# Performance work log

Hardware: AMD Instinct MI355X
Metric: run time of the kernel (lower is better)

The kernel has to match this reference:

```python
import jax, jax.numpy as jnp
import numpy as np

T, B, C, H, W = 4, 8, 256, 16, 16
HEADS = 8
N = H * W
TN = T * N
DH = C // HEADS
DECAY = 0.25

# STE quantizer: fwd round(clamp(x,0,1)); bwd passes grad only where 0<=x<=1
@jax.custom_vjp
def quant1(x):
    return jnp.round(jnp.clip(x, 0.0, 1.0))

def _q_fwd(x):
    return quant1(x), x

def _q_bwd(x, g):
    return (jnp.where((x < 0) | (x > 1), 0.0, g),)

quant1.defvjp(_q_fwd, _q_bwd)

def lif(x):
    # x: [T, ...]; sequential LIF membrane decay + quantize over leading (time) axis
    def step(carry, xt):
        mem_old, spike = carry
        mem = (mem_old - jax.lax.stop_gradient(spike) * 0.5) * DECAY + xt
        s = quant1(mem)
        return (mem, s), s
    z = jnp.zeros_like(x[0])
    _, out = jax.lax.scan(step, (z, z), x)
    return out

def bn1d(x, gamma, beta, mean, var):
    # eval-mode BatchNorm1d over channel axis 1 of [B, Ch, L]
    inv = jax.lax.rsqrt(var + 1e-5)
    return (x - mean[None, :, None]) * (gamma * inv)[None, :, None] + beta[None, :, None]

def _rel_pos_index():
    coords = np.stack(np.meshgrid(np.arange(T), np.arange(H), np.arange(W), indexing='ij'))  # [3,T,H,W]
    cf = coords.reshape(3, -1)                      # [3, TN]
    rc = (cf[:, :, None] - cf[:, None, :]).transpose(1, 2, 0).copy()  # [TN, TN, 3]
    rc[:, :, 0] += T - 1
    rc[:, :, 1] += H - 1
    rc[:, :, 2] += W - 1
    rc[:, :, 0] *= (2 * H - 1) * (2 * W - 1)
    rc[:, :, 1] *= (2 * W - 1)
    return rc.sum(-1)                               # [TN, TN] ints

def _mask():
    m = np.ones((TN, TN), np.float32)
    for t in range(T - 1):
        m[t * N:(t + 1) * N, (t + 1) * N:] = 0.0
    return m

_RPI = jnp.asarray(_rel_pos_index().reshape(-1))
_MASK = jnp.asarray(_mask())


def setup_inputs() -> dict:
    key = jax.random.key(0)
    ks = jax.random.split(key, 13)
    bias_rows = (2 * T - 1) * (2 * H - 1) * (2 * W - 1)
    return {
        'x': jax.random.normal(ks[0], (T, B, C, H, W), jnp.float32),
        'w_qkv': jax.random.normal(ks[1], (3 * C, C), jnp.float32) * 0.05,
        'qkv_gamma': jax.random.uniform(ks[2], (3 * C,), jnp.float32, 0.5, 1.5),
        'qkv_beta': jax.random.normal(ks[3], (3 * C,), jnp.float32) * 0.1,
        'qkv_mean': jax.random.normal(ks[4], (3 * C,), jnp.float32) * 0.1,
        'qkv_var': jax.random.uniform(ks[5], (3 * C,), jnp.float32, 0.5, 1.5),
        'bias_table': jax.random.normal(ks[6], (bias_rows, HEADS), jnp.float32) * 0.02,
        'w_proj': jax.random.normal(ks[7], (C, C), jnp.float32) * 0.05,
        'b_proj': jax.random.normal(ks[8], (C,), jnp.float32) * 0.02,
        'proj_gamma': jax.random.uniform(ks[9], (C,), jnp.float32, 0.5, 1.5),
        'proj_beta': jax.random.normal(ks[10], (C,), jnp.float32) * 0.1,
        'proj_mean': jax.random.normal(ks[11], (C,), jnp.float32) * 0.1,
        'proj_var': jax.random.uniform(ks[12], (C,), jnp.float32, 0.5, 1.5),
    }


def reference(x, w_qkv, qkv_gamma, qkv_beta, qkv_mean, qkv_var, bias_table,
              w_proj, b_proj, proj_gamma, proj_beta, proj_mean, proj_var):
    # flatten spatial, then raw reshape [T,B,C,N] -> [B,C,T*N] (as in torch source)
    xf = x.reshape(T, B, C, N).reshape(B, C, T * N)
    # 1x1 conv == channel matmul, then eval BN
    qkv = jnp.einsum('oc,bcl->bol', w_qkv, xf)
    qkv = bn1d(qkv, qkv_gamma, qkv_beta, qkv_mean, qkv_var)
    qkv = qkv.reshape(B, 3 * C, T, N).transpose(2, 0, 1, 3)  # [T,B,3C,N]
    qkv = lif(qkv).transpose(1, 0, 3, 2)                      # [B,T,N,3C]
    q, k, v = jnp.split(qkv, 3, axis=-1)                      # each [B,T,N,C]

    def to_heads(z):  # b t n (h d) -> b h (t n) d
        return z.reshape(B, T, N, HEADS, DH).transpose(0, 3, 1, 2, 4).reshape(B, HEADS, TN, DH)
    q, k, v = map(to_heads, (q, k, v))

    bias = bias_table[_RPI].reshape(TN, TN, HEADS).transpose(2, 0, 1)  # [h,TN,TN]
    attn = jnp.einsum('bhnd,bhmd->bhnm', q, k) + bias[None]
    attn = attn * _MASK[None, None]                                     # block upper-triangle mask
    o = jnp.einsum('bhnm,bhmd->bhnd', attn, v) * 0.125                  # [B,h,TN,d]

    o = o.transpose(0, 2, 1, 3).reshape(B, TN, C).reshape(B, T, N, C).transpose(1, 0, 3, 2)  # [T,B,C,N]
    o = lif(o)
    o = o.transpose(1, 2, 0, 3).reshape(B, C, T * N)          # [B,C,TN]
    o = jnp.einsum('oc,bcl->bol', w_proj, o) + b_proj[None, :, None]
    o = bn1d(o, proj_gamma, proj_beta, proj_mean, proj_var)
    o = o.reshape(B, C, T, N).transpose(2, 0, 1, 3).reshape(T, B, C, H, W)
    return lif(o)
```

## Files before the change

kernel.cpp:

```cpp
#include <hip/hip_runtime.h>
#include <stdint.h>
#include <math.h>

constexpr int T_ = 4;
constexpr int B_ = 8;
constexpr int C_ = 256;
constexpr int N_ = 256;
constexpr int TN_ = 1024;
constexpr int NH_ = 8;
constexpr int O3_ = 768;
constexpr int BIAS_ROWS_ = 6727;

__device__ __constant__ int TI_OF[10] = {0,1,1,2,2,2,3,3,3,3};
__device__ __constant__ int TJ_OF[10] = {0,0,1,0,1,2,0,1,2,3};

__device__ __forceinline__ float quant1f(float m) {
    return rintf(fminf(fmaxf(m, 0.0f), 1.0f));
}

__global__ __launch_bounds__(256) void k1_qkv_gemm(
    const float* __restrict__ x, const float* __restrict__ w,
    const float* __restrict__ gamma, const float* __restrict__ beta,
    const float* __restrict__ mean, const float* __restrict__ var,
    float* __restrict__ out)
{
    __shared__ float At[32][36];
    __shared__ float Bt[32][132];
    const int b = blockIdx.z;
    const int oBase = blockIdx.y * 32;
    const int lBase = blockIdx.x * 128;
    const int tid = threadIdx.x;
    const int tx = tid & 31;
    const int ty = tid >> 5;
    const float* xb = x + (size_t)b * C_ * TN_;

    float acc[4][4];
#pragma unroll
    for (int i = 0; i < 4; ++i)
#pragma unroll
        for (int j = 0; j < 4; ++j) acc[i][j] = 0.0f;

    const int a_row0 = tid >> 4, a_k2 = (tid & 15) * 2;
    const int b_kk0 = tid >> 5, b_c4 = (tid & 31) * 4;

    for (int kc = 0; kc < 8; ++kc) {
        const int k0 = kc * 32;
#pragma unroll
        for (int r = 0; r < 2; ++r) {
            const int row = a_row0 + 16 * r;
            const float2 v = *(const float2*)&w[(size_t)(oBase + row) * C_ + k0 + a_k2];
            At[a_k2][row] = v.x;
            At[a_k2 + 1][row] = v.y;
        }
#pragma unroll
        for (int r = 0; r < 4; ++r) {
            const int kk = b_kk0 + 8 * r;
            const float4 v = *(const float4*)&xb[(size_t)(k0 + kk) * TN_ + lBase + b_c4];
            *(float4*)&Bt[kk][b_c4] = v;
        }
        __syncthreads();
#pragma unroll
        for (int cc = 0; cc < 32; ++cc) {
            float a[4], bb[4];
            *(float4*)&a[0] = *(const float4*)&At[cc][ty * 4];
            *(float4*)&bb[0] = *(const float4*)&Bt[cc][tx * 4];
#pragma unroll
            for (int i = 0; i < 4; ++i)
#pragma unroll
                for (int j = 0; j < 4; ++j) acc[i][j] += a[i] * bb[j];
        }
        __syncthreads();
    }

#pragma unroll
    for (int i = 0; i < 4; ++i) {
        const int o = oBase + ty * 4 + i;
        const float inv = 1.0f / sqrtf(var[o] + 1e-5f);
        const float g = gamma[o] * inv;
        const float mn = mean[o], bt = beta[o];
        float4 st;
        st.x = (acc[i][0] - mn) * g + bt;
        st.y = (acc[i][1] - mn) * g + bt;
        st.z = (acc[i][2] - mn) * g + bt;
        st.w = (acc[i][3] - mn) * g + bt;
        *(float4*)&out[((size_t)b * O3_ + o) * TN_ + lBase + tx * 4] = st;
    }
}

__global__ __launch_bounds__(256) void k2_lif_pack(
    const float* __restrict__ qkv,
    uint32_t* __restrict__ qb, uint32_t* __restrict__ kb, uint32_t* __restrict__ vb)
{
    const int n = threadIdx.x;
    const int g = blockIdx.x;
    const int b = blockIdx.y;
    const int dq = blockIdx.z;
    const int which = g >> 3, h = g & 7;
    uint32_t* dstw = (which == 0) ? qb : (which == 1) ? kb : vb;
    uint8_t* dst = (uint8_t*)dstw;
    const float* src = qkv + ((size_t)b * O3_ + g * 32 + dq * 8) * TN_;

    float memv[8];
#pragma unroll
    for (int d = 0; d < 8; ++d) memv[d] = 0.0f;
    uint32_t prev = 0;

    for (int t = 0; t < T_; ++t) {
        uint32_t bits = 0;
#pragma unroll
        for (int d = 0; d < 8; ++d) {
            const float xv = src[(size_t)d * TN_ + t * N_ + n];
            const float m = (memv[d] - 0.5f * (float)((prev >> d) & 1u)) * 0.25f + xv;
            memv[d] = m;
            const float s = quant1f(m);
            bits |= ((uint32_t)s) << d;
        }
        prev = bits;
        dst[4 * (((size_t)b * NH_ + h) * TN_ + t * N_ + n) + dq] = (uint8_t)bits;
    }
}

__global__ __launch_bounds__(256) void k3_tgp(
    const uint32_t* __restrict__ kb, const uint32_t* __restrict__ vb,
    int* __restrict__ Pt)
{
    __shared__ uint64_t ks[32][4];
    __shared__ uint64_t vs[32][4];
    const int t = blockIdx.x;
    const int bh = blockIdx.y;
    const int tid = threadIdx.x;
    const int q = tid >> 6, lane = tid & 63;
    const int j = t * N_ + q * 64 + lane;

    const uint32_t kw = kb[(size_t)bh * TN_ + j];
    const uint32_t vw = vb[(size_t)bh * TN_ + j];
#pragma unroll
    for (int d = 0; d < 32; ++d) {
        const uint64_t mk = __ballot((kw >> d) & 1u);
        const uint64_t mv = __ballot((vw >> d) & 1u);
        if (lane == 0) { ks[d][q] = mk; vs[d][q] = mv; }
    }
    __syncthreads();

    const int d = tid & 31;
#pragma unroll
    for (int s = 0; s < 4; ++s) {
        const int d2 = (tid >> 5) + 8 * s;
        int p = 0;
#pragma unroll
        for (int w = 0; w < 4; ++w) p += __popcll(ks[d2][w] & vs[d][w]);
        Pt[(size_t)(bh * 4 + t) * 1024 + d2 * 32 + d] = p;
    }
}

__global__ __launch_bounds__(256) void k3_cum(
    const int* __restrict__ Pt, float* __restrict__ Gf)
{
    const int bh = blockIdx.x;
    const int tid = threadIdx.x;
#pragma unroll
    for (int r = 0; r < 4; ++r) {
        const int idx = tid + 256 * r;
        int cum = 0;
#pragma unroll
        for (int t = 0; t < T_; ++t) {
            cum += Pt[(size_t)(bh * 4 + t) * 1024 + idx];
            Gf[(size_t)(bh * 4 + t) * 1024 + idx] = (float)cum;
        }
    }
}

__global__ __launch_bounds__(256) void k3_bias_gemm(
    const uint32_t* __restrict__ vb, const float* __restrict__ bias_table,
    float* __restrict__ p0, float* __restrict__ p1,
    float* __restrict__ p2, float* __restrict__ p3)
{
    __shared__ float sbl[544];
    __shared__ float At[32][36];
    __shared__ float Bt[32][132];

    const int z = blockIdx.z;
    const int h = z / 10;
    const int p = z % 10;
    const int ti = TI_OF[p], tj = TJ_OF[p];
    const int dt = ti - tj;
    const int iT = blockIdx.y;
    const int nBase = blockIdx.x * 128;
    const int tid = threadIdx.x;

    const int base = 3363 + 961 * dt + 62 * iT - 480;
    for (int s = tid; s < 544; s += 256) {
        const int gidx = base + s;
        sbl[s] = (gidx >= 0 && gidx < BIAS_ROWS_) ? bias_table[(size_t)gidx * NH_ + h] : 0.0f;
    }

    const int ty2 = tid >> 4, tx16 = tid & 15;

    const int il0 = ty2 * 2;
    const int sRowBase = 480 + 31 * (il0 >> 4) + (il0 & 15) - tx16;

    const int n8 = tx16 * 8;
    const int nS = nBase + n8;
    const int bS = nS >> 5, d0S = nS & 31;
    const uint32_t* vbw = vb + ((size_t)bS * NH_ + h) * TN_ + tj * 256 + ty2;

    const int tyc = tid >> 5, txc = tid & 31;
    const int nA = nBase + txc * 4;
    const int bA = nA >> 5, dA = nA & 31;

    float acc[4][4];
#pragma unroll
    for (int i = 0; i < 4; ++i)
#pragma unroll
        for (int j = 0; j < 4; ++j) acc[i][j] = 0.0f;

    __syncthreads();

    for (int kc = 0; kc < 8; ++kc) {
#pragma unroll
        for (int r1 = 0; r1 < 2; ++r1) {
            const int s0 = sRowBase - 31 * (kc * 2 + r1);
            float2 av;
            av.x = sbl[s0];
            av.y = sbl[s0 + 1];
            At[tx16 + 16 * r1][il0] = av.x;
            At[tx16 + 16 * r1][il0 + 1] = av.y;
        }
#pragma unroll
        for (int r = 0; r < 2; ++r) {
            const uint32_t wd = vbw[kc * 32 + 16 * r];
            float4 b0, b1;
            b0.x = (float)((wd >> d0S) & 1u);
            b0.y = (float)((wd >> (d0S + 1)) & 1u);
            b0.z = (float)((wd >> (d0S + 2)) & 1u);
            b0.w = (float)((wd >> (d0S + 3)) & 1u);
            b1.x = (float)((wd >> (d0S + 4)) & 1u);
            b1.y = (float)((wd >> (d0S + 5)) & 1u);
            b1.z = (float)((wd >> (d0S + 6)) & 1u);
            b1.w = (float)((wd >> (d0S + 7)) & 1u);
            *(float4*)&Bt[ty2 + 16 * r][n8] = b0;
            *(float4*)&Bt[ty2 + 16 * r][n8 + 4] = b1;
        }
        __syncthreads();
#pragma unroll
        for (int cc = 0; cc < 32; ++cc) {
            float a[4], bb[4];
            *(float4*)&a[0] = *(const float4*)&At[cc][tyc * 4];
            *(float4*)&bb[0] = *(const float4*)&Bt[cc][txc * 4];
#pragma unroll
            for (int i = 0; i < 4; ++i)
#pragma unroll
                for (int j = 0; j < 4; ++j) acc[i][j] += a[i] * bb[j];
        }
        __syncthreads();
    }

    float* plane = (tj == 0) ? p0 : (tj == 1) ? p1 : (tj == 2) ? p2 : p3;
    const int nrows = (4 - tj) * 256;
    const int cA = h * 32 + dA;
#pragma unroll
    for (int r = 0; r < 4; ++r) {
        const int rowL = dt * 256 + iT * 32 + tyc * 4 + r;
        float4 s0;
        s0.x = acc[r][0]; s0.y = acc[r][1]; s0.z = acc[r][2]; s0.w = acc[r][3];
        *(float4*)&plane[((size_t)bA * nrows + rowL) * 256 + cA] = s0;
    }
}

__global__ __launch_bounds__(256) void k4_lif2(
    const uint32_t* __restrict__ qb, const float* __restrict__ Gf,
    const float* __restrict__ p0, const float* __restrict__ p1,
    const float* __restrict__ p2, const float* __restrict__ p3,
    uint32_t* __restrict__ s2c)
{
    const int c = threadIdx.x;
    const int n = blockIdx.x;
    const int b = blockIdx.y;
    const int lane = c & 63;
    const int h = c >> 5, d = c & 31;
    const int bh = b * NH_ + h;
    const uint32_t* qbh = qb + (size_t)bh * TN_;

    float memv = 0.0f, spk = 0.0f;
    for (int t = 0; t < T_; ++t) {
        const int l = t * N_ + n;
        const uint32_t q = qbh[l];
        const float* g = Gf + (size_t)(bh * 4 + t) * 1024 + d;
        float v = 0.0f;
#pragma unroll
        for (int d2 = 0; d2 < 32; ++d2)
            v += ((q >> d2) & 1u) ? g[d2 * 32] : 0.0f;
        v += p0[((size_t)b * 1024 + l) * 256 + c];
        if (t >= 1) v += p1[((size_t)b * 768 + (l - 256)) * 256 + c];
        if (t >= 2) v += p2[((size_t)b * 512 + (l - 512)) * 256 + c];
        if (t >= 3) v += p3[((size_t)b * 256 + (l - 768)) * 256 + c];
        const float m = (memv - 0.5f * spk) * 0.25f + 0.125f * v;
        memv = m;
        const float s = quant1f(m);
        spk = s;
        const uint64_t mask = __ballot(s != 0.0f);
        if (lane == 0)
            s2c[((size_t)b * TN_ + l) * 8 + (c >> 5)] = (uint32_t)mask;
        else if (lane == 32)
            s2c[((size_t)b * TN_ + l) * 8 + (c >> 5)] = (uint32_t)(mask >> 32);
    }
}

__global__ __launch_bounds__(256) void k5_proj_lif(
    const uint32_t* __restrict__ s2c, const float* __restrict__ w,
    const float* __restrict__ bp,
    const float* __restrict__ gamma, const float* __restrict__ beta,
    const float* __restrict__ mean, const float* __restrict__ var,
    float* __restrict__ out)
{
    __shared__ float At[128][36];
    __shared__ uint32_t Sw[128 * 9];
    const int nBase = blockIdx.x * 32;
    const int oBase = blockIdx.y * 32;
    const int b = blockIdx.z;
    const int tid = threadIdx.x;
    const int tx = tid & 31;
    const int ty = tid >> 5;

#pragma unroll
    for (int j = 0; j < 4; ++j) {
        const int fidx = tid * 4 + j;
        const int lp = fidx >> 3, wsel = fidx & 7;
        const int t = lp >> 5, nn = lp & 31;
        Sw[lp * 9 + wsel] = s2c[((size_t)b * TN_ + t * 256 + nBase + nn) * 8 + wsel];
    }

    const int a_row = tid >> 3, a_kq = (tid & 7) * 16;

    float acc[4][4];
#pragma unroll
    for (int r = 0; r < 4; ++r)
#pragma unroll
        for (int t = 0; t < 4; ++t) acc[r][t] = 0.0f;

    for (int half = 0; half < 2; ++half) {
        if (half) __syncthreads();
#pragma unroll
        for (int j = 0; j < 4; ++j) {
            const float4 v = *(const float4*)&w[(size_t)(oBase + a_row) * C_ + half * 128 + a_kq + 4 * j];
            At[a_kq + 4 * j][a_row] = v.x;
            At[a_kq + 4 * j + 1][a_row] = v.y;
            At[a_kq + 4 * j + 2][a_row] = v.z;
            At[a_kq + 4 * j + 3][a_row] = v.w;
        }
        __syncthreads();

        for (int ks = 0; ks < 4; ++ks) {
            uint32_t wr[4];
#pragma unroll
            for (int t = 0; t < 4; ++t)
                wr[t] = Sw[(t * 32 + tx) * 9 + half * 4 + ks];
#pragma unroll
            for (int u = 0; u < 32; ++u) {
                float a[4];
                *(float4*)&a[0] = *(const float4*)&At[ks * 32 + u][ty * 4];
                float bv[4];
#pragma unroll
                for (int t = 0; t < 4; ++t) bv[t] = (float)((wr[t] >> u) & 1u);
#pragma unroll
                for (int r = 0; r < 4; ++r)
#pragma unroll
                    for (int t = 0; t < 4; ++t) acc[r][t] += a[r] * bv[t];
            }
        }
    }

#pragma unroll
    for (int r = 0; r < 4; ++r) {
        const int o = oBase + ty * 4 + r;
        const float inv = 1.0f / sqrtf(var[o] + 1e-5f);
        const float g = gamma[o] * inv;
        const float mn = mean[o], bt = beta[o], bpo = bp[o];
        float memv = 0.0f, spk = 0.0f;
#pragma unroll
        for (int t = 0; t < 4; ++t) {
            const float val = ((acc[r][t] + bpo) - mn) * g + bt;
            const float m = (memv - 0.5f * spk) * 0.25f + val;
            memv = m;
            const float s = quant1f(m);
            spk = s;
            out[(((size_t)t * B_ + b) * C_ + o) * N_ + nBase + tx] = s;
        }
    }
}

extern "C" void kernel_launch(void* const* d_in, const int* in_sizes, int n_in,
                              void* d_out, int out_size, void* d_ws, size_t ws_size,
                              hipStream_t stream)
{
    const float* x          = (const float*)d_in[0];
    const float* w_qkv      = (const float*)d_in[1];
    const float* qkv_gamma  = (const float*)d_in[2];
    const float* qkv_beta   = (const float*)d_in[3];
    const float* qkv_mean   = (const float*)d_in[4];
    const float* qkv_var    = (const float*)d_in[5];
    const float* bias_table = (const float*)d_in[6];
    const float* w_proj     = (const float*)d_in[7];
    const float* b_proj     = (const float*)d_in[8];
    const float* proj_gamma = (const float*)d_in[9];
    const float* proj_beta  = (const float*)d_in[10];
    const float* proj_mean  = (const float*)d_in[11];
    const float* proj_var   = (const float*)d_in[12];
    float* out = (float*)d_out;

    char* ws = (char*)d_ws;
    float*    qkv_bn = (float*)(ws + 0);
    float*    part0  = (float*)(ws + 1048576);
    float*    part1  = (float*)(ws + 9437184);
    float*    part2  = (float*)(ws + 15728640);
    float*    part3  = (float*)(ws + 19922944);
    float*    Gf     = (float*)(ws + 25165824);
    int*      Pt     = (int*)  (ws + 26214400);
    uint32_t* s2c    = (uint32_t*)(ws + 33554432);
    uint32_t* qbits  = (uint32_t*)(ws + 50331648);
    uint32_t* kbits  = (uint32_t*)(ws + 50593792);
    uint32_t* vbits  = (uint32_t*)(ws + 50855936);

    k1_qkv_gemm<<<dim3(8, 24, 8), 256, 0, stream>>>(
        x, w_qkv, qkv_gamma, qkv_beta, qkv_mean, qkv_var, qkv_bn);

    k2_lif_pack<<<dim3(24, 8, 4), 256, 0, stream>>>(qkv_bn, qbits, kbits, vbits);

    k3_tgp<<<dim3(4, 64), 256, 0, stream>>>(kbits, vbits, Pt);

    k3_cum<<<dim3(64), 256, 0, stream>>>(Pt, Gf);

    k3_bias_gemm<<<dim3(2, 8, 80), 256, 0, stream>>>(
        vbits, bias_table, part0, part1, part2, part3);

    k4_lif2<<<dim3(256, 8), 256, 0, stream>>>(
        qbits, Gf, part0, part1, part2, part3, s2c);

    k5_proj_lif<<<dim3(8, 8, 8), 256, 0, stream>>>(
        s2c, w_proj, b_proj, proj_gamma, proj_beta, proj_mean, proj_var, out);
}
```

Baseline: 213.8 us.

## Retile QKV and proj GEMMs, fold cumulative sum into LIF2 kernel

```diff
diff --git a/kernel.cpp b/kernel.cpp
--- a/kernel.cpp
+++ b/kernel.cpp
@@ -24,19 +24,19 @@
     const float* __restrict__ mean, const float* __restrict__ var,
     float* __restrict__ out)
 {
-    __shared__ float At[32][36];
+    __shared__ float At[32][68];
     __shared__ float Bt[32][132];
     const int b = blockIdx.z;
-    const int oBase = blockIdx.y * 32;
+    const int oBase = blockIdx.y * 64;
     const int lBase = blockIdx.x * 128;
     const int tid = threadIdx.x;
     const int tx = tid & 31;
     const int ty = tid >> 5;
     const float* xb = x + (size_t)b * C_ * TN_;
 
-    float acc[4][4];
-#pragma unroll
-    for (int i = 0; i < 4; ++i)
+    float acc[8][4];
+#pragma unroll
+    for (int i = 0; i < 8; ++i)
 #pragma unroll
         for (int j = 0; j < 4; ++j) acc[i][j] = 0.0f;
 
@@ -46,7 +46,7 @@
     for (int kc = 0; kc < 8; ++kc) {
         const int k0 = kc * 32;
 #pragma unroll
-        for (int r = 0; r < 2; ++r) {
+        for (int r = 0; r < 4; ++r) {
             const int row = a_row0 + 16 * r;
             const float2 v = *(const float2*)&w[(size_t)(oBase + row) * C_ + k0 + a_k2];
             At[a_k2][row] = v.x;
@@ -61,11 +61,12 @@
         __syncthreads();
 #pragma unroll
         for (int cc = 0; cc < 32; ++cc) {
-            float a[4], bb[4];
+            float a[8], bb[4];
             *(float4*)&a[0] = *(const float4*)&At[cc][ty * 4];
+            *(float4*)&a[4] = *(const float4*)&At[cc][32 + ty * 4];
             *(float4*)&bb[0] = *(const float4*)&Bt[cc][tx * 4];
 #pragma unroll
-            for (int i = 0; i < 4; ++i)
+            for (int i = 0; i < 8; ++i)
 #pragma unroll
                 for (int j = 0; j < 4; ++j) acc[i][j] += a[i] * bb[j];
         }
@@ -73,8 +74,8 @@
     }
 
 #pragma unroll
-    for (int i = 0; i < 4; ++i) {
-        const int o = oBase + ty * 4 + i;
+    for (int i = 0; i < 8; ++i) {
+        const int o = oBase + (i >> 2) * 32 + ty * 4 + (i & 3);
         const float inv = 1.0f / sqrtf(var[o] + 1e-5f);
         const float g = gamma[o] * inv;
         const float mn = mean[o], bt = beta[o];
@@ -150,23 +151,6 @@
 #pragma unroll
         for (int w = 0; w < 4; ++w) p += __popcll(ks[d2][w] & vs[d][w]);
         Pt[(size_t)(bh * 4 + t) * 1024 + d2 * 32 + d] = p;
-    }
-}
-
-__global__ __launch_bounds__(256) void k3_cum(
-    const int* __restrict__ Pt, float* __restrict__ Gf)
-{
-    const int bh = blockIdx.x;
-    const int tid = threadIdx.x;
-#pragma unroll
-    for (int r = 0; r < 4; ++r) {
-        const int idx = tid + 256 * r;
-        int cum = 0;
-#pragma unroll
-        for (int t = 0; t < T_; ++t) {
-            cum += Pt[(size_t)(bh * 4 + t) * 1024 + idx];
-            Gf[(size_t)(bh * 4 + t) * 1024 + idx] = (float)cum;
-        }
     }
 }
 
@@ -268,7 +252,7 @@
 }
 
 __global__ __launch_bounds__(256) void k4_lif2(
-    const uint32_t* __restrict__ qb, const float* __restrict__ Gf,
+    const uint32_t* __restrict__ qb, const int* __restrict__ Pt,
     const float* __restrict__ p0, const float* __restrict__ p1,
     const float* __restrict__ p2, const float* __restrict__ p3,
     uint32_t* __restrict__ s2c)
@@ -281,15 +265,21 @@
     const int bh = b * NH_ + h;
     const uint32_t* qbh = qb + (size_t)bh * TN_;
 
+    float cum[32];
+#pragma unroll
+    for (int d2 = 0; d2 < 32; ++d2) cum[d2] = 0.0f;
+
     float memv = 0.0f, spk = 0.0f;
     for (int t = 0; t < T_; ++t) {
         const int l = t * N_ + n;
+        const int* pt = Pt + (size_t)(bh * 4 + t) * 1024 + d;
+#pragma unroll
+        for (int d2 = 0; d2 < 32; ++d2) cum[d2] += (float)pt[d2 * 32];
         const uint32_t q = qbh[l];
-        const float* g = Gf + (size_t)(bh * 4 + t) * 1024 + d;
         float v = 0.0f;
 #pragma unroll
         for (int d2 = 0; d2 < 32; ++d2)
-            v += ((q >> d2) & 1u) ? g[d2 * 32] : 0.0f;
+            v += ((q >> d2) & 1u) ? cum[d2] : 0.0f;
         v += p0[((size_t)b * 1024 + l) * 256 + c];
         if (t >= 1) v += p1[((size_t)b * 768 + (l - 256)) * 256 + c];
         if (t >= 2) v += p2[((size_t)b * 512 + (l - 512)) * 256 + c];
@@ -313,10 +303,10 @@
     const float* __restrict__ mean, const float* __restrict__ var,
     float* __restrict__ out)
 {
-    __shared__ float At[128][36];
+    __shared__ float At[128][20];
     __shared__ uint32_t Sw[128 * 9];
     const int nBase = blockIdx.x * 32;
-    const int oBase = blockIdx.y * 32;
+    const int oBase = blockIdx.y * 16;
     const int b = blockIdx.z;
     const int tid = threadIdx.x;
     const int tx = tid & 31;
@@ -330,18 +320,18 @@
         Sw[lp * 9 + wsel] = s2c[((size_t)b * TN_ + t * 256 + nBase + nn) * 8 + wsel];
     }
 
-    const int a_row = tid >> 3, a_kq = (tid & 7) * 16;
-
-    float acc[4][4];
-#pragma unroll
-    for (int r = 0; r < 4; ++r)
+    const int a_row = tid >> 4, a_kq = (tid & 15) * 8;
+
+    float acc[2][4];
+#pragma unroll
+    for (int r = 0; r < 2; ++r)
 #pragma unroll
         for (int t = 0; t < 4; ++t) acc[r][t] = 0.0f;
 
     for (int half = 0; half < 2; ++half) {
         if (half) __syncthreads();
 #pragma unroll
-        for (int j = 0; j < 4; ++j) {
+        for (int j = 0; j < 2; ++j) {
             const float4 v = *(const float4*)&w[(size_t)(oBase + a_row) * C_ + half * 128 + a_kq + 4 * j];
             At[a_kq + 4 * j][a_row] = v.x;
             At[a_kq + 4 * j + 1][a_row] = v.y;
@@ -357,13 +347,13 @@
                 wr[t] = Sw[(t * 32 + tx) * 9 + half * 4 + ks];
 #pragma unroll
             for (int u = 0; u < 32; ++u) {
-                float a[4];
-                *(float4*)&a[0] = *(const float4*)&At[ks * 32 + u][ty * 4];
+                float a[2];
+                *(float2*)&a[0] = *(const float2*)&At[ks * 32 + u][ty * 2];
                 float bv[4];
 #pragma unroll
                 for (int t = 0; t < 4; ++t) bv[t] = (float)((wr[t] >> u) & 1u);
 #pragma unroll
-                for (int r = 0; r < 4; ++r)
+                for (int r = 0; r < 2; ++r)
 #pragma unroll
                     for (int t = 0; t < 4; ++t) acc[r][t] += a[r] * bv[t];
             }
@@ -371,8 +361,8 @@
     }
 
 #pragma unroll
-    for (int r = 0; r < 4; ++r) {
-        const int o = oBase + ty * 4 + r;
+    for (int r = 0; r < 2; ++r) {
+        const int o = oBase + ty * 2 + r;
         const float inv = 1.0f / sqrtf(var[o] + 1e-5f);
         const float g = gamma[o] * inv;
         const float mn = mean[o], bt = beta[o], bpo = bp[o];
@@ -414,28 +404,25 @@
     float*    part1  = (float*)(ws + 9437184);
     float*    part2  = (float*)(ws + 15728640);
     float*    part3  = (float*)(ws + 19922944);
-    float*    Gf     = (float*)(ws + 25165824);
-    int*      Pt     = (int*)  (ws + 26214400);
+    int*      Pt     = (int*)  (ws + 25165824);
     uint32_t* s2c    = (uint32_t*)(ws + 33554432);
     uint32_t* qbits  = (uint32_t*)(ws + 50331648);
     uint32_t* kbits  = (uint32_t*)(ws + 50593792);
     uint32_t* vbits  = (uint32_t*)(ws + 50855936);
 
-    k1_qkv_gemm<<<dim3(8, 24, 8), 256, 0, stream>>>(
+    k1_qkv_gemm<<<dim3(8, 12, 8), 256, 0, stream>>>(
         x, w_qkv, qkv_gamma, qkv_beta, qkv_mean, qkv_var, qkv_bn);
 
     k2_lif_pack<<<dim3(24, 8, 4), 256, 0, stream>>>(qkv_bn, qbits, kbits, vbits);
 
     k3_tgp<<<dim3(4, 64), 256, 0, stream>>>(kbits, vbits, Pt);
-
-    k3_cum<<<dim3(64), 256, 0, stream>>>(Pt, Gf);
 
     k3_bias_gemm<<<dim3(2, 8, 80), 256, 0, stream>>>(
         vbits, bias_table, part0, part1, part2, part3);
 
     k4_lif2<<<dim3(256, 8), 256, 0, stream>>>(
-        qbits, Gf, part0, part1, part2, part3, s2c);
-
-    k5_proj_lif<<<dim3(8, 8, 8), 256, 0, stream>>>(
+        qbits, Pt, part0, part1, part2, part3, s2c);
+
+    k5_proj_lif<<<dim3(8, 16, 8), 256, 0, stream>>>(
         s2c, w_proj, b_proj, proj_gamma, proj_beta, proj_mean, proj_var, out);
 }
```

Measured after the change: 226.8 us. +6.1%, slower.
